# Kernel tuning notes

Hardware: AMD Instinct MI355X
Metric: run time of the kernel (lower is better)

Reference implementation:

```python
import jax, jax.numpy as jnp
import numpy as np

NUM_BATCH, NUM_OBJ, NUM_DBOX, NUM_CLASSES = 64, 50, 8732, 2
JACCARD_THRESH = 0.5
NEGPOS_RATIO = 3
VARIANCE = (0.1, 0.2)


def setup_inputs() -> dict:
    key = jax.random.key(0)
    k1, k2, k3, k4, k5, k6 = jax.random.split(key, 6)
    loc_data = jax.random.normal(k1, (NUM_BATCH, NUM_DBOX, 4), dtype=jnp.float32)
    conf_data = jax.random.normal(k2, (NUM_BATCH, NUM_DBOX, NUM_CLASSES), dtype=jnp.float32)
    # default boxes in center-size form (cx, cy, w, h)
    cxcy = jax.random.uniform(k3, (NUM_DBOX, 2), minval=0.05, maxval=0.95)
    wh = jax.random.uniform(k4, (NUM_DBOX, 2), minval=0.05, maxval=0.4)
    dbox_list = jnp.concatenate([cxcy, wh], axis=1).astype(jnp.float32)
    # ground-truth boxes in point form [xmin,ymin,xmax,ymax] plus label (class 0 -> conf label 1)
    tc = jax.random.uniform(k5, (NUM_BATCH, NUM_OBJ, 2), minval=0.15, maxval=0.85)
    twh = jax.random.uniform(k6, (NUM_BATCH, NUM_OBJ, 2), minval=0.05, maxval=0.3)
    truths = jnp.concatenate([tc - twh / 2, tc + twh / 2], axis=-1)
    labels = jnp.zeros((NUM_BATCH, NUM_OBJ, 1), dtype=jnp.float32)
    targets = jnp.concatenate([truths, labels], axis=-1).astype(jnp.float32)
    return {"loc_data": loc_data, "conf_data": conf_data, "dbox_list": dbox_list, "targets": targets}


def point_form(boxes):
    # (cx,cy,w,h) -> (xmin,ymin,xmax,ymax)
    return jnp.concatenate([boxes[:, :2] - boxes[:, 2:] / 2, boxes[:, :2] + boxes[:, 2:] / 2], axis=1)


def jaccard(a, b):
    # a: [No,4], b: [Nd,4], both point form -> [No,Nd]
    lt = jnp.maximum(a[:, None, :2], b[None, :, :2])
    rb = jnp.minimum(a[:, None, 2:], b[None, :, 2:])
    wh = jnp.clip(rb - lt, 0.0)
    inter = wh[..., 0] * wh[..., 1]
    area_a = ((a[:, 2] - a[:, 0]) * (a[:, 3] - a[:, 1]))[:, None]
    area_b = ((b[:, 2] - b[:, 0]) * (b[:, 3] - b[:, 1]))[None, :]
    return inter / (area_a + area_b - inter)


def encode(matched, priors):
    # matched: [Nd,4] point form; priors: [Nd,4] center-size form
    g_cxcy = (matched[:, :2] + matched[:, 2:]) / 2 - priors[:, :2]
    g_cxcy = g_cxcy / (VARIANCE[0] * priors[:, 2:])
    g_wh = jnp.log((matched[:, 2:] - matched[:, :2]) / priors[:, 2:]) / VARIANCE[1]
    return jnp.concatenate([g_cxcy, g_wh], axis=1)


def match_one(truths, labels, dbox):
    # truths [No,4], labels [No], dbox [Nd,4] center-size
    overlaps = jaccard(truths, point_form(dbox))  # [No, Nd]
    best_prior_idx = jnp.argmax(overlaps, axis=1)          # [No]
    best_truth_overlap = jnp.max(overlaps, axis=0)          # [Nd]
    best_truth_idx = jnp.argmax(overlaps, axis=0)           # [Nd]
    best_truth_overlap = best_truth_overlap.at[best_prior_idx].set(2.0)
    best_truth_idx = best_truth_idx.at[best_prior_idx].set(jnp.arange(truths.shape[0]))
    matched = truths[best_truth_idx]                        # [Nd,4]
    conf = labels[best_truth_idx].astype(jnp.int32) + 1
    conf = jnp.where(best_truth_overlap < JACCARD_THRESH, 0, conf)
    loc = encode(matched, dbox)
    return loc, conf


def smooth_l1(x, t):
    d = jnp.abs(x - t)
    return jnp.where(d < 1.0, 0.5 * d * d, d - 0.5)


def cross_entropy(logits, labels):
    # logits [..., C], labels [...] int -> elementwise CE
    logp = jax.nn.log_softmax(logits, axis=-1)
    return -jnp.take_along_axis(logp, labels[..., None], axis=-1)[..., 0]


def reference(loc_data, conf_data, dbox_list, targets):
    num_batch, num_dbox, _ = loc_data.shape
    truths = targets[..., :-1]        # [B,No,4]
    labels = targets[..., -1]          # [B,No]
    loc_t, conf_t_label = jax.vmap(match_one, in_axes=(0, 0, None))(truths, labels, dbox_list)
    pos_mask = conf_t_label > 0        # [B,Nd]

    # localization loss: smooth L1 over positive priors, mean over selected elements
    l1 = smooth_l1(loc_data, loc_t)                               # [B,Nd,4]
    n_pos_elems = 4.0 * jnp.sum(pos_mask)
    loss_l = jnp.nan_to_num(jnp.sum(l1 * pos_mask[..., None]) / n_pos_elems)

    # per-prior confidence loss for hard-negative mining
    ce = cross_entropy(conf_data, conf_t_label)                   # [B,Nd]
    ce_mined = jnp.where(pos_mask, 0.0, ce)
    loss_idx = jnp.argsort(-ce_mined, axis=1)                     # descending sort
    idx_rank = jnp.argsort(loss_idx, axis=1)
    num_pos = jnp.sum(pos_mask, axis=1, keepdims=True)            # [B,1]
    num_neg = jnp.clip(num_pos * NEGPOS_RATIO, 20, num_dbox)
    neg_mask = idx_rank < num_neg                                 # [B,Nd]

    posf = pos_mask.astype(ce.dtype)
    negf = neg_mask.astype(ce.dtype)
    loss_c_pos = jnp.nan_to_num(jnp.sum(ce * posf) / jnp.sum(posf))
    loss_c_neg = jnp.nan_to_num(jnp.sum(ce * negf) / jnp.sum(negf))
    loss_c = loss_c_pos + loss_c_neg
    return jnp.stack([loss_l, loss_c, loss_c_pos, loss_c_neg])
```

## Files before the change

kernel.cpp:

```cpp
#include <hip/hip_runtime.h>

#define NB     64
#define NOBJ   50
#define ND     8732
#define PPT    3
#define BLK1   256
#define PRB    (BLK1*PPT)
#define NSPLIT 12
#define NW1    (BLK1/64)
#define NPART  (NSPLIT*NW1)
#define CHUNK  10
#define NCHUNK 5
#define BLK2   1024
#define NW2    (BLK2/64)
#define ITER2  ((ND+BLK2-1)/BLK2)
#define ND4    (ND/4)

__device__ float              g_part[NB*5];
__device__ float4             g_ce4[(size_t)NB*ND4];
__device__ unsigned long long g_keys[(size_t)NB*NPART*NOBJ];
__device__ int                g_hist[(size_t)NB*NSPLIT*256];
__device__ float              g_bp[NB*NSPLIT*3];
__device__ int                g_done;

__device__ __forceinline__ float iou_rn(float px1,float py1,float px2,float py2,float pa,
                                        float tx1,float ty1,float tx2,float ty2,float ta){
    float ltx=fmaxf(tx1,px1), lty=fmaxf(ty1,py1);
    float rbx=fminf(tx2,px2), rby=fminf(ty2,py2);
    float ww=fmaxf(__fsub_rn(rbx,ltx),0.f), hh=fmaxf(__fsub_rn(rby,lty),0.f);
    float inter=__fmul_rn(ww,hh);
    return __fdividef(inter, __fsub_rn(__fadd_rn(ta,pa),inter));
}
__device__ __forceinline__ float lse2(float x0,float x1){
    float m=fmaxf(x0,x1);
    return m+__logf(__expf(x0-m)+__expf(x1-m));
}
__device__ __forceinline__ float sl1_enc(float4 p,float tx1,float ty1,float tx2,float ty2,float4 ld){
    float g0=((tx1+tx2)*0.5f-p.x)/(0.1f*p.z);
    float g1=((ty1+ty2)*0.5f-p.y)/(0.1f*p.w);
    float g2=__logf((tx2-tx1)/p.z)*5.0f;
    float g3=__logf((ty2-ty1)/p.w)*5.0f;
    float t0=fabsf(ld.x-g0),t1=fabsf(ld.y-g1),t2=fabsf(ld.z-g2),t3=fabsf(ld.w-g3);
    return (t0<1.f?0.5f*t0*t0:t0-0.5f)+(t1<1.f?0.5f*t1*t1:t1-0.5f)
          +(t2<1.f?0.5f*t2*t2:t2-0.5f)+(t3<1.f?0.5f*t3*t3:t3-0.5f);
}

__global__ __launch_bounds__(BLK1) void k1(const float* __restrict__ loc_data,
                                           const float* __restrict__ conf_data,
                                           const float* __restrict__ dbox,
                                           const float* __restrict__ targets){
    __shared__ float s_tx1[NOBJ],s_ty1[NOBJ],s_tx2[NOBJ],s_ty2[NOBJ],s_ta[NOBJ],s_lab[NOBJ];
    __shared__ int   s_wh[NW1*256];
    __shared__ float s_r1[NW1],s_r2[NW1],s_r3[NW1];
    const int blk=blockIdx.x, b=blk/NSPLIT, spl=blk%NSPLIT;
    const int tid=threadIdx.x, lane=tid&63, wv=tid>>6;
    if (blk==0 && tid==0) g_done=0;
    if (tid<NOBJ){
        const float* t=targets+(b*NOBJ+tid)*5;
        float x1=t[0],y1=t[1],x2=t[2],y2=t[3];
        s_tx1[tid]=x1;s_ty1[tid]=y1;s_tx2[tid]=x2;s_ty2[tid]=y2;
        s_ta[tid]=__fmul_rn(__fsub_rn(x2,x1),__fsub_rn(y2,y1));
        s_lab[tid]=t[4];
    }
    for (int i=tid;i<NW1*256;i+=BLK1) s_wh[i]=0;
    __syncthreads();

    const int d0=spl*PRB;
    const int cnt=(ND-d0<PRB)?(ND-d0):PRB;
    float px1[PPT],py1[PPT],px2[PPT],py2[PPT],pa[PPT];
    bool vld[PPT]; float bov[PPT]; int bj[PPT];
#pragma unroll
    for (int q=0;q<PPT;++q){
        int dl=tid*PPT+q; vld[q]=dl<cnt; bov[q]=-1.f; bj[q]=0;
        px1[q]=py1[q]=px2[q]=py2[q]=pa[q]=0.f;
        if (vld[q]){
            float4 p=reinterpret_cast<const float4*>(dbox)[d0+dl];
            float hw=__fmul_rn(0.5f,p.z), hh=__fmul_rn(0.5f,p.w);
            px1[q]=__fsub_rn(p.x,hw); py1[q]=__fsub_rn(p.y,hh);
            px2[q]=__fadd_rn(p.x,hw); py2[q]=__fadd_rn(p.y,hh);
            pa[q]=__fmul_rn(p.z,p.w);
        }
    }
    unsigned long long* kout=g_keys+(((size_t)b*NSPLIT+spl)*NW1+wv)*NOBJ;

    for (int c=0;c<NCHUNK;++c){
        float tx1c[CHUNK],ty1c[CHUNK],tx2c[CHUNK],ty2c[CHUNK],tac[CHUNK];
#pragma unroll
        for (int jj=0;jj<CHUNK;++jj){int j=c*CHUNK+jj;
            tx1c[jj]=s_tx1[j];ty1c[jj]=s_ty1[j];tx2c[jj]=s_tx2[j];ty2c[jj]=s_ty2[j];tac[jj]=s_ta[j];}
        float tb[CHUNK]; int td[CHUNK];
#pragma unroll
        for (int jj=0;jj<CHUNK;++jj){tb[jj]=-1.f;td[jj]=0;}
#pragma unroll
        for (int q=0;q<PPT;++q){
            if (!vld[q]) continue;
            const int d=d0+tid*PPT+q;
#pragma unroll
            for (int jj=0;jj<CHUNK;++jj){
                float iou=iou_rn(px1[q],py1[q],px2[q],py2[q],pa[q],
                                 tx1c[jj],ty1c[jj],tx2c[jj],ty2c[jj],tac[jj]);
                if (iou>bov[q]){bov[q]=iou;bj[q]=c*CHUNK+jj;}
                if (iou>tb[jj]){tb[jj]=iou;td[jj]=d;}
            }
        }
#pragma unroll
        for (int jj=0;jj<CHUNK;++jj){
            float m=tb[jj];
#pragma unroll
            for (int off=32;off>=1;off>>=1) m=fmaxf(m,__shfl_xor(m,off,64));
            unsigned long long msk=__ballot(tb[jj]==m);
            int lead=__builtin_ctzll(msk);
            int dwin=__shfl(td[jj],lead,64);
            if (lane==0){
                unsigned long long enc=(m>=0.f)
                    ?(((unsigned long long)__float_as_uint(m)<<32)
                      |(unsigned long long)(0xFFFFFFFFu-(unsigned)dwin))
                    :0ull;
                kout[c*CHUNK+jj]=enc;
            }
        }
    }

    float* gce=(float*)g_ce4;
    float np=0.f,sl=0.f,sc=0.f;
#pragma unroll
    for (int q=0;q<PPT;++q){
        if (!vld[q]) continue;
        const int d=d0+tid*PPT+q;
        float2 cf=reinterpret_cast<const float2*>(conf_data)[(size_t)b*ND+d];
        float l=lse2(cf.x,cf.y);
        bool pos=!(bov[q]<0.5f);
        int jb=bj[q];
        int lab=pos?((int)s_lab[jb]+1):0;
        float cev=l-(lab>=1?cf.y:cf.x);
        float raw=pos?-cev:cev;
        gce[(size_t)b*ND+d]=raw;
        atomicAdd(&s_wh[wv*256+(int)(__float_as_uint(fmaxf(raw,0.f))>>24)],1);
        if (pos){
            np+=1.f; sc+=cev;
            float4 p=reinterpret_cast<const float4*>(dbox)[d];
            float4 ldv=reinterpret_cast<const float4*>(loc_data)[(size_t)b*ND+d];
            sl+=sl1_enc(p,s_tx1[jb],s_ty1[jb],s_tx2[jb],s_ty2[jb],ldv);
        }
    }
#pragma unroll
    for (int off=32;off>=1;off>>=1){
        np+=__shfl_xor(np,off,64); sl+=__shfl_xor(sl,off,64); sc+=__shfl_xor(sc,off,64);
    }
    if (lane==0){s_r1[wv]=np;s_r2[wv]=sl;s_r3[wv]=sc;}
    __syncthreads();
    if (tid==0){
        float a=0.f,bb2=0.f,cc=0.f;
        for (int w=0;w<NW1;++w){a+=s_r1[w];bb2+=s_r2[w];cc+=s_r3[w];}
        g_bp[(b*NSPLIT+spl)*3+0]=a;
        g_bp[(b*NSPLIT+spl)*3+1]=bb2;
        g_bp[(b*NSPLIT+spl)*3+2]=cc;
    }
    {
        int s=0;
        for (int w=0;w<NW1;++w) s+=s_wh[w*256+tid];
        g_hist[(size_t)(b*NSPLIT+spl)*256+tid]=s;
    }
}

__global__ __launch_bounds__(BLK2) void k2(const float* __restrict__ loc_data,
                                           const float* __restrict__ conf_data,
                                           const float* __restrict__ dbox,
                                           const float* __restrict__ targets,
                                           float* __restrict__ out){
    __shared__ float4 s_ce4[ND4];
    __shared__ unsigned long long s_km[NOBJ*16];
    __shared__ unsigned int s_dj[NOBJ];
    __shared__ float s_tx1[NOBJ],s_ty1[NOBJ],s_tx2[NOBJ],s_ty2[NOBJ],s_ta[NOBJ],s_lab[NOBJ];
    __shared__ int   s_hist[256];
    __shared__ int   s_wh[NW2*256];
    __shared__ float s_bpl[NSPLIT*3];
    __shared__ float s_rf[NW2]; __shared__ int s_ri[NW2];
    __shared__ int   s_wt[4];
    __shared__ float s_dnp,s_dsl,s_dsc;
    __shared__ int   s_sel,s_krem,s_kk,s_last;
    float* s_ce=(float*)s_ce4;

    const int b=blockIdx.x, tid=threadIdx.x, lane=tid&63, wv=tid>>6;

    if (tid<NOBJ){
        const float* t=targets+(b*NOBJ+tid)*5;
        float x1=t[0],y1=t[1],x2=t[2],y2=t[3];
        s_tx1[tid]=x1;s_ty1[tid]=y1;s_tx2[tid]=x2;s_ty2[tid]=y2;
        s_ta[tid]=__fmul_rn(__fsub_rn(x2,x1),__fsub_rn(y2,y1));
        s_lab[tid]=t[4];
    }
    if (tid<NOBJ*16){
        int j=tid>>4, s=tid&15;
        const unsigned long long* kp=g_keys+(size_t)b*NPART*NOBJ;
        unsigned long long m=kp[(size_t)s*NOBJ+j];
        unsigned long long o=kp[(size_t)(s+16)*NOBJ+j]; if(o>m)m=o;
        o=kp[(size_t)(s+32)*NOBJ+j]; if(o>m)m=o;
        s_km[tid]=m;
    }
    for (int i=tid;i<ND4;i+=BLK2) s_ce4[i]=g_ce4[(size_t)b*ND4+i];
    if (tid<256){
        int s=0;
        for (int sp=0;sp<NSPLIT;++sp) s+=g_hist[(size_t)(b*NSPLIT+sp)*256+tid];
        s_hist[tid]=s;
    }
    if (tid<NSPLIT*3) s_bpl[tid]=g_bp[b*NSPLIT*3+tid];
    __syncthreads();
    if (tid<NOBJ){
        unsigned long long m=s_km[tid*16];
        for (int s=1;s<16;++s){unsigned long long o=s_km[tid*16+s]; if(o>m)m=o;}
        s_dj[tid]=0xFFFFFFFFu-(unsigned)(m&0xFFFFFFFFull);
    }
    __syncthreads();

    float dnp=0.f,dsl=0.f,dsc=0.f;
    if (tid<NOBJ){
        unsigned d=s_dj[tid]; bool win=true;
        for (int j2=tid+1;j2<NOBJ;++j2) if (s_dj[j2]==d){win=false;break;}
        if (win){
            float4 p=reinterpret_cast<const float4*>(dbox)[d];
            float hw=__fmul_rn(0.5f,p.z), hh2=__fmul_rn(0.5f,p.w);
            float ppx1=__fsub_rn(p.x,hw),ppy1=__fsub_rn(p.y,hh2);
            float ppx2=__fadd_rn(p.x,hw),ppy2=__fadd_rn(p.y,hh2);
            float ppa=__fmul_rn(p.z,p.w);
            float bov=-1.f; int jb=0;
            for (int j=0;j<NOBJ;++j){
                float iou=iou_rn(ppx1,ppy1,ppx2,ppy2,ppa,
                                 s_tx1[j],s_ty1[j],s_tx2[j],s_ty2[j],s_ta[j]);
                if (iou>bov){bov=iou;jb=j;}
            }
            bool oldpos=!(bov<0.5f);
            float2 cf=reinterpret_cast<const float2*>(conf_data)[(size_t)b*ND+d];
            float l=lse2(cf.x,cf.y);
            float4 ldv=reinterpret_cast<const float4*>(loc_data)[(size_t)b*ND+d];
            int labN=(int)s_lab[tid]+1;
            float ceN=l-(labN>=1?cf.y:cf.x);
            dsc+=ceN; dsl+=sl1_enc(p,s_tx1[tid],s_ty1[tid],s_tx2[tid],s_ty2[tid],ldv);
            if (oldpos){
                int labO=(int)s_lab[jb]+1;
                float ceO=l-(labO>=1?cf.y:cf.x);
                dsc-=ceO; dsl-=sl1_enc(p,s_tx1[jb],s_ty1[jb],s_tx2[jb],s_ty2[jb],ldv);
            } else dnp+=1.f;
            float oldraw=s_ce[d];
            atomicAdd(&s_hist[(int)(__float_as_uint(fmaxf(oldraw,0.f))>>24)],-1);
            atomicAdd(&s_hist[0],1);
            s_ce[d]=-ceN;
        }
    }
    if (wv==0){
#pragma unroll
        for (int off=32;off>=1;off>>=1){
            dnp+=__shfl_xor(dnp,off,64); dsl+=__shfl_xor(dsl,off,64); dsc+=__shfl_xor(dsc,off,64);
        }
        if (lane==0){s_dnp=dnp;s_dsl=dsl;s_dsc=dsc;}
    }
    __syncthreads();
    if (tid==0){
        float np=s_dnp, sl=s_dsl, sc=s_dsc;
        for (int i=0;i<NSPLIT;++i){np+=s_bpl[i*3];sl+=s_bpl[i*3+1];sc+=s_bpl[i*3+2];}
        int npi=(int)np; int k=npi*3; if(k<20)k=20; if(k>ND)k=ND;
        s_kk=k;
        g_part[b*5+0]=np; g_part[b*5+1]=sl; g_part[b*5+2]=sc; g_part[b*5+3]=(float)k;
    }
    __syncthreads();
    const int k=s_kk;

    unsigned prefix=0u,pmask=0u; int krem=k;
    for (int p=0;p<3;++p){
        const int shift=24-p*8;
        int cnt=0;
        if (p==0){
            if (tid<256) cnt=s_hist[tid];
        } else {
            for (int i=tid;i<NW2*256;i+=BLK2) s_wh[i]=0;
            __syncthreads();
            for (int it=0;it<ITER2;++it){
                int d=tid+it*BLK2;
                if (d<ND){
                    unsigned vb=__float_as_uint(fmaxf(s_ce[d],0.f));
                    if ((vb&pmask)==prefix)
                        atomicAdd(&s_wh[wv*256+(int)((vb>>shift)&255u)],1);
                }
            }
            __syncthreads();
            if (tid<256){
                for (int w=0;w<NW2;++w) cnt+=s_wh[w*256+tid];
            }
        }
        int S=cnt,add=0;
        if (tid<256){
#pragma unroll
            for (int off=1;off<64;off<<=1){
                int t=__shfl_down(S,off,64);
                if (lane+off<64) S+=t;
            }
            if (lane==0) s_wt[wv]=S;
        }
        __syncthreads();
        if (tid<256){
            for (int w=wv+1;w<4;++w) add+=s_wt[w];
            S+=add;
            int Snext=__shfl_down(S,1,64);
            if (lane==63) Snext=add;
            if (S>=krem && Snext<krem){s_sel=tid;s_krem=krem-(S-cnt);}
        }
        __syncthreads();
        prefix|=((unsigned)s_sel)<<shift;
        pmask|=255u<<shift;
        krem=s_krem;
        __syncthreads();
    }
    const float T=__uint_as_float(prefix);

    int cgt=0; float sgt=0.f;
    for (int it=0;it<ITER2;++it){
        int d=tid+it*BLK2;
        if (d<ND){
            float v=fmaxf(s_ce[d],0.f);
            if (v>T){cgt++;sgt+=v;}
        }
    }
#pragma unroll
    for (int off=32;off>=1;off>>=1){cgt+=__shfl_xor(cgt,off,64);sgt+=__shfl_xor(sgt,off,64);}
    if (lane==0){s_ri[wv]=cgt;s_rf[wv]=sgt;}
    __syncthreads();
    if (tid==0){
        int cg=0; float sg=0.f;
        for (int w=0;w<NW2;++w){cg+=s_ri[w];sg+=s_rf[w];}
        int need=k-cg;
        float stk=sg+(float)need*T;
        if (!(T>0.f)&&need>0){
            int taken=0;
            for (int d=0;d<ND&&taken<need;++d){
                float r=s_ce[d];
                if (!(r>0.f)){stk+=fabsf(r);++taken;}
            }
        }
        g_part[b*5+4]=stk;
    }

    if (tid==0){__threadfence(); int old=atomicAdd(&g_done,1); s_last=(old==NB-1)?1:0;}
    __syncthreads();
    if (s_last&&tid<NB){
        __threadfence();
        volatile float* gp=g_part;
        float np=gp[tid*5+0],sl=gp[tid*5+1],sc=gp[tid*5+2],kk=gp[tid*5+3],st=gp[tid*5+4];
#pragma unroll
        for (int off=32;off>=1;off>>=1){
            np+=__shfl_xor(np,off,64);sl+=__shfl_xor(sl,off,64);
            sc+=__shfl_xor(sc,off,64);kk+=__shfl_xor(kk,off,64);st+=__shfl_xor(st,off,64);
        }
        if (tid==0){
            float loss_l=(np>0.f)?sl/(4.f*np):0.f;
            float lcp=(np>0.f)?sc/np:0.f;
            float lcn=(kk>0.f)?st/kk:0.f;
            out[0]=loss_l;out[1]=lcp+lcn;out[2]=lcp;out[3]=lcn;
        }
    }
}

extern "C" void kernel_launch(void* const* d_in, const int* in_sizes, int n_in,
                              void* d_out, int out_size, void* d_ws, size_t ws_size,
                              hipStream_t stream) {
    const float* loc     = (const float*)d_in[0];
    const float* conf    = (const float*)d_in[1];
    const float* dboxp   = (const float*)d_in[2];
    const float* targets = (const float*)d_in[3];
    float* out = (float*)d_out;

    k1<<<NB*NSPLIT, BLK1, 0, stream>>>(loc, conf, dboxp, targets);
    k2<<<NB, BLK2, 0, stream>>>(loc, conf, dboxp, targets, out);
}
```

Measured before the change: 123.5 us.

## Split priors across more blocks and reduce match keys per block in shared memory

Cuts priors per thread from three to two and raises the per-image split from 12 to 18, which gives more, lighter blocks for the matching kernel. Per-wave best-prior keys are now max-reduced in shared memory before one global write per block, which shrinks the key buffer and the reduction work in the second kernel. Confidence inputs and cross-entropy outputs move as one float4 load and one float2 store per thread, and target coordinates and areas are read straight from global memory per chunk instead of being staged in shared memory. The trade-off is an extra block-level barrier and repeated target loads and area computation in every chunk.

```diff
diff --git a/kernel.cpp b/kernel.cpp
--- a/kernel.cpp
+++ b/kernel.cpp
@@ -3,12 +3,12 @@
 #define NB     64
 #define NOBJ   50
 #define ND     8732
-#define PPT    3
+#define PPT    2
 #define BLK1   256
 #define PRB    (BLK1*PPT)
-#define NSPLIT 12
+#define NSPLIT 18
 #define NW1    (BLK1/64)
-#define NPART  (NSPLIT*NW1)
+#define NPART  NSPLIT
 #define CHUNK  10
 #define NCHUNK 5
 #define BLK2   1024
@@ -49,7 +49,8 @@
                                            const float* __restrict__ conf_data,
                                            const float* __restrict__ dbox,
                                            const float* __restrict__ targets){
-    __shared__ float s_tx1[NOBJ],s_ty1[NOBJ],s_tx2[NOBJ],s_ty2[NOBJ],s_ta[NOBJ],s_lab[NOBJ];
+    __shared__ float s_tx1[NOBJ],s_ty1[NOBJ],s_tx2[NOBJ],s_ty2[NOBJ],s_lab[NOBJ];
+    __shared__ unsigned long long s_wk[NW1][NOBJ];
     __shared__ int   s_wh[NW1*256];
     __shared__ float s_r1[NW1],s_r2[NW1],s_r3[NW1];
     const int blk=blockIdx.x, b=blk/NSPLIT, spl=blk%NSPLIT;
@@ -57,13 +58,9 @@
     if (blk==0 && tid==0) g_done=0;
     if (tid<NOBJ){
         const float* t=targets+(b*NOBJ+tid)*5;
-        float x1=t[0],y1=t[1],x2=t[2],y2=t[3];
-        s_tx1[tid]=x1;s_ty1[tid]=y1;s_tx2[tid]=x2;s_ty2[tid]=y2;
-        s_ta[tid]=__fmul_rn(__fsub_rn(x2,x1),__fsub_rn(y2,y1));
-        s_lab[tid]=t[4];
+        s_tx1[tid]=t[0];s_ty1[tid]=t[1];s_tx2[tid]=t[2];s_ty2[tid]=t[3];s_lab[tid]=t[4];
     }
     for (int i=tid;i<NW1*256;i+=BLK1) s_wh[i]=0;
-    __syncthreads();
 
     const int d0=spl*PRB;
     const int cnt=(ND-d0<PRB)?(ND-d0):PRB;
@@ -81,13 +78,17 @@
             pa[q]=__fmul_rn(p.z,p.w);
         }
     }
-    unsigned long long* kout=g_keys+(((size_t)b*NSPLIT+spl)*NW1+wv)*NOBJ;
-
+
+    const float* tg = targets + (size_t)b*NOBJ*5;
     for (int c=0;c<NCHUNK;++c){
         float tx1c[CHUNK],ty1c[CHUNK],tx2c[CHUNK],ty2c[CHUNK],tac[CHUNK];
 #pragma unroll
-        for (int jj=0;jj<CHUNK;++jj){int j=c*CHUNK+jj;
-            tx1c[jj]=s_tx1[j];ty1c[jj]=s_ty1[j];tx2c[jj]=s_tx2[j];ty2c[jj]=s_ty2[j];tac[jj]=s_ta[j];}
+        for (int jj=0;jj<CHUNK;++jj){
+            int j=c*CHUNK+jj;
+            tx1c[jj]=tg[j*5+0]; ty1c[jj]=tg[j*5+1];
+            tx2c[jj]=tg[j*5+2]; ty2c[jj]=tg[j*5+3];
+            tac[jj]=__fmul_rn(__fsub_rn(tx2c[jj],tx1c[jj]),__fsub_rn(ty2c[jj],ty1c[jj]));
+        }
         float tb[CHUNK]; int td[CHUNK];
 #pragma unroll
         for (int jj=0;jj<CHUNK;++jj){tb[jj]=-1.f;td[jj]=0;}
@@ -112,36 +113,44 @@
             int lead=__builtin_ctzll(msk);
             int dwin=__shfl(td[jj],lead,64);
             if (lane==0){
-                unsigned long long enc=(m>=0.f)
+                s_wk[wv][c*CHUNK+jj]=(m>=0.f)
                     ?(((unsigned long long)__float_as_uint(m)<<32)
                       |(unsigned long long)(0xFFFFFFFFu-(unsigned)dwin))
                     :0ull;
-                kout[c*CHUNK+jj]=enc;
-            }
-        }
-    }
-
-    float* gce=(float*)g_ce4;
+            }
+        }
+    }
+    __syncthreads();
+    if (tid<NOBJ){
+        unsigned long long m=s_wk[0][tid];
+        for (int w=1;w<NW1;++w){unsigned long long o=s_wk[w][tid]; if(o>m)m=o;}
+        g_keys[((size_t)b*NSPLIT+spl)*NOBJ+tid]=m;
+    }
+
     float np=0.f,sl=0.f,sc=0.f;
-#pragma unroll
-    for (int q=0;q<PPT;++q){
-        if (!vld[q]) continue;
-        const int d=d0+tid*PPT+q;
-        float2 cf=reinterpret_cast<const float2*>(conf_data)[(size_t)b*ND+d];
-        float l=lse2(cf.x,cf.y);
-        bool pos=!(bov[q]<0.5f);
-        int jb=bj[q];
-        int lab=pos?((int)s_lab[jb]+1):0;
-        float cev=l-(lab>=1?cf.y:cf.x);
-        float raw=pos?-cev:cev;
-        gce[(size_t)b*ND+d]=raw;
-        atomicAdd(&s_wh[wv*256+(int)(__float_as_uint(fmaxf(raw,0.f))>>24)],1);
-        if (pos){
-            np+=1.f; sc+=cev;
-            float4 p=reinterpret_cast<const float4*>(dbox)[d];
-            float4 ldv=reinterpret_cast<const float4*>(loc_data)[(size_t)b*ND+d];
-            sl+=sl1_enc(p,s_tx1[jb],s_ty1[jb],s_tx2[jb],s_ty2[jb],ldv);
-        }
+    float raw[PPT]={0.f,0.f};
+    if (vld[0]){
+        float4 cf4=reinterpret_cast<const float4*>(conf_data)[((size_t)b*ND+d0)/2+tid];
+#pragma unroll
+        for (int q=0;q<PPT;++q){
+            const int d=d0+tid*PPT+q;
+            float cfx=(q==0)?cf4.x:cf4.z, cfy=(q==0)?cf4.y:cf4.w;
+            float l=lse2(cfx,cfy);
+            bool pos=!(bov[q]<0.5f);
+            int jb=bj[q];
+            int lab=pos?((int)s_lab[jb]+1):0;
+            float cev=l-(lab>=1?cfy:cfx);
+            raw[q]=pos?-cev:cev;
+            atomicAdd(&s_wh[wv*256+(int)(__float_as_uint(fmaxf(raw[q],0.f))>>24)],1);
+            if (pos){
+                np+=1.f; sc+=cev;
+                float4 p=reinterpret_cast<const float4*>(dbox)[d];
+                float4 ldv=reinterpret_cast<const float4*>(loc_data)[(size_t)b*ND+d];
+                sl+=sl1_enc(p,s_tx1[jb],s_ty1[jb],s_tx2[jb],s_ty2[jb],ldv);
+            }
+        }
+        float2 st; st.x=raw[0]; st.y=raw[1];
+        reinterpret_cast<float2*>(g_ce4)[((size_t)b*ND+d0)/2+tid]=st;
     }
 #pragma unroll
     for (int off=32;off>=1;off>>=1){
@@ -194,8 +203,7 @@
         int j=tid>>4, s=tid&15;
         const unsigned long long* kp=g_keys+(size_t)b*NPART*NOBJ;
         unsigned long long m=kp[(size_t)s*NOBJ+j];
-        unsigned long long o=kp[(size_t)(s+16)*NOBJ+j]; if(o>m)m=o;
-        o=kp[(size_t)(s+32)*NOBJ+j]; if(o>m)m=o;
+        if (s+16<NPART){unsigned long long o=kp[(size_t)(s+16)*NOBJ+j]; if(o>m)m=o;}
         s_km[tid]=m;
     }
     for (int i=tid;i<ND4;i+=BLK2) s_ce4[i]=g_ce4[(size_t)b*ND4+i];
```

Result: slower. 136.9 us (+10.9%).
